# Optimization experiments

Measured on AMD Instinct MI355X. Metric: run time of the kernel, lower is better.

The kernel has to match this reference:

```python
import jax, jax.numpy as jnp
import numpy as np


def setup_inputs() -> dict:
    key = jax.random.key(0)
    x = jax.random.normal(key, (2_000_000, 9), dtype=jnp.float32)
    return {"x": x}


def reference(x):
    # Symmetric orthogonalization onto SO(3):
    #   M = U S V^T ;  R = U diag(1, 1, det(U V^T)) V^T
    m = x.reshape(-1, 3, 3)                      # [N, 3, 3]
    u, s, vh = jnp.linalg.svd(m, full_matrices=False)  # u:[N,3,3], vh:[N,3,3] (= V^T)
    det = jnp.linalg.det(jnp.matmul(u, vh))      # [N]
    # Flip last column of U by sign of det to land in SO(3) (det = +1)
    u_fixed = jnp.concatenate(
        [u[:, :, :2], u[:, :, 2:] * det[:, None, None]], axis=2
    )
    return jnp.matmul(u_fixed, vh)               # [N, 3, 3]
```

## Files before the change

kernel.cpp:

```cpp
#include <hip/hip_runtime.h>

#define TPB 256
#define MPW 128
#define FPW (MPW * 9)

typedef float v2f __attribute__((ext_vector_type(2)));
typedef int   v2i __attribute__((ext_vector_type(2)));

static __device__ __forceinline__ v2f sqrt2(v2f a){
    v2f r; r.x = __builtin_amdgcn_sqrtf(a.x); r.y = __builtin_amdgcn_sqrtf(a.y); return r;
}
static __device__ __forceinline__ v2f rsq2(v2f a){
    v2f r; r.x = __builtin_amdgcn_rsqf(a.x); r.y = __builtin_amdgcn_rsqf(a.y); return r;
}
static __device__ __forceinline__ v2f csign2(v2f x, v2f y){
    v2f r; r.x = copysignf(x.x, y.x); r.y = copysignf(x.y, y.y); return r;
}
static __device__ __forceinline__ v2f fabs2(v2f x){
    v2f r; r.x = fabsf(x.x); r.y = fabsf(x.y); return r;
}
static __device__ __forceinline__ v2f sel2(v2i m, v2f a, v2f b){
    v2f r; r.x = m.x ? a.x : b.x; r.y = m.y ? a.y : b.y; return r;
}
static __device__ __forceinline__ void rot2(v2f &p, v2f &q, v2f c, v2f s){
    v2f x = p, y = q; p = c*x - s*y; q = s*x + c*y;
}

static __device__ __forceinline__ void jrot2(v2f &app, v2f &aqq, v2f &apq,
                                             v2f &arp, v2f &arq,
                                             v2f &v0p, v2f &v1p, v2f &v2p,
                                             v2f &v0q, v2f &v1q, v2f &v2q)
{
    v2f d   = aqq - app;
    v2f w   = apq + apq;
    v2f nrm = d*d + w*w;
    v2f rr  = sqrt2(nrm);
    v2f sr  = csign2(rr, d);
    v2f den = d + sr;
    v2f inv = rsq2(den*den + w*w);
    v2f c   = fabs2(den) * inv;
    v2f s   = w * csign2(inv, den);
    v2i tiny = nrm < (v2f)1e-30f;
    c = sel2(tiny, (v2f)1.0f, c);
    s = sel2(tiny, (v2f)0.0f, s);
    v2f sum = app + aqq;
    v2f lo  = 0.5f*(sum - sr);
    app = lo; aqq = sum - lo; apq = (v2f)0.0f;
    rot2(arp, arq, c, s);
    rot2(v0p, v0q, c, s);
    rot2(v1p, v1q, c, s);
    rot2(v2p, v2q, c, s);
}

static __device__ __forceinline__ void solve2(
    v2f m00, v2f m01, v2f m02,
    v2f m10, v2f m11, v2f m12,
    v2f m20, v2f m21, v2f m22,
    v2f &r00, v2f &r01, v2f &r02,
    v2f &r10, v2f &r11, v2f &r12,
    v2f &r20, v2f &r21, v2f &r22)
{
    v2f a00 = m00*m00 + m10*m10 + m20*m20;
    v2f a11 = m01*m01 + m11*m11 + m21*m21;
    v2f a22 = m02*m02 + m12*m12 + m22*m22;
    v2f a01 = m00*m01 + m10*m11 + m20*m21;
    v2f a02 = m00*m02 + m10*m12 + m20*m22;
    v2f a12 = m01*m02 + m11*m12 + m21*m22;

    v2f v00 = (v2f)1.0f, v01 = (v2f)0.0f, v02 = (v2f)0.0f;
    v2f v10 = (v2f)0.0f, v11 = (v2f)1.0f, v12 = (v2f)0.0f;
    v2f v20 = (v2f)0.0f, v21 = (v2f)0.0f, v22 = (v2f)1.0f;

    #pragma unroll
    for (int sw = 0; sw < 3; ++sw) {
        jrot2(a00, a11, a01, a02, a12, v00, v10, v20, v01, v11, v21);
        jrot2(a00, a22, a02, a01, a12, v00, v10, v20, v02, v12, v22);
        jrot2(a11, a22, a12, a01, a02, v01, v11, v21, v02, v12, v22);
    }

    v2f t;
    {
        v2i c01 = a00 < a11;
        t = a00; a00 = sel2(c01, a11, a00); a11 = sel2(c01, t, a11);
        t = v00; v00 = sel2(c01, v01, v00); v01 = sel2(c01, -t, v01);
        t = v10; v10 = sel2(c01, v11, v10); v11 = sel2(c01, -t, v11);
        t = v20; v20 = sel2(c01, v21, v20); v21 = sel2(c01, -t, v21);
    }
    {
        v2i c02 = a00 < a22;
        t = a00; a00 = sel2(c02, a22, a00); a22 = sel2(c02, t, a22);
        t = v00; v00 = sel2(c02, v02, v00); v02 = sel2(c02, -t, v02);
        t = v10; v10 = sel2(c02, v12, v10); v12 = sel2(c02, -t, v12);
        t = v20; v20 = sel2(c02, v22, v20); v22 = sel2(c02, -t, v22);
    }
    {
        v2i c12 = a11 < a22;
        t = a11; a11 = sel2(c12, a22, a11); a22 = sel2(c12, t, a22);
        t = v01; v01 = sel2(c12, v02, v01); v02 = sel2(c12, -t, v02);
        t = v11; v11 = sel2(c12, v12, v11); v12 = sel2(c12, -t, v12);
        t = v21; v21 = sel2(c12, v22, v21); v22 = sel2(c12, -t, v22);
    }

    v2f b00 = m00*v00 + m01*v10 + m02*v20;
    v2f b10 = m10*v00 + m11*v10 + m12*v20;
    v2f b20 = m20*v00 + m21*v10 + m22*v20;
    v2f b01 = m00*v01 + m01*v11 + m02*v21;
    v2f b11 = m10*v01 + m11*v11 + m12*v21;
    v2f b21 = m20*v01 + m21*v11 + m22*v21;

    v2f n1 = b00*b00 + b10*b10 + b20*b20;
    v2f i1 = rsq2(n1);
    v2i ok1 = n1 > (v2f)1e-30f;
    i1 = sel2(ok1, i1, (v2f)0.0f);
    v2f u00 = b00*i1, u10 = b10*i1, u20 = b20*i1;

    v2f d12 = b01*u00 + b11*u10 + b21*u20;
    v2f q0 = b01 - d12*u00;
    v2f q1 = b11 - d12*u10;
    v2f q2 = b21 - d12*u20;
    v2f n2 = q0*q0 + q1*q1 + q2*q2;
    v2f i2 = rsq2(n2);
    v2i ok2 = n2 > (v2f)1e-30f;
    i2 = sel2(ok2, i2, (v2f)0.0f);
    v2f u01 = q0*i2, u11 = q1*i2, u21 = q2*i2;

    v2f u02 = u10*u21 - u20*u11;
    v2f u12 = u20*u01 - u00*u21;
    v2f u22 = u00*u11 - u10*u01;

    r00 = u00*v00 + u01*v01 + u02*v02;
    r01 = u00*v10 + u01*v11 + u02*v12;
    r02 = u00*v20 + u01*v21 + u02*v22;
    r10 = u10*v00 + u11*v01 + u12*v02;
    r11 = u10*v10 + u11*v11 + u12*v12;
    r12 = u10*v20 + u11*v21 + u12*v22;
    r20 = u20*v00 + u21*v01 + u22*v02;
    r21 = u20*v10 + u21*v11 + u22*v12;
    r22 = u20*v20 + u21*v21 + u22*v22;
}

static __device__ __forceinline__ float4 ld_f4(const float* __restrict__ x, long f, long ntotf){
    if (f + 4 <= ntotf) return *(const float4*)(x + f);
    float4 r = make_float4(0.f, 0.f, 0.f, 0.f);
    if (f     < ntotf) r.x = x[f];
    if (f + 1 < ntotf) r.y = x[f + 1];
    if (f + 2 < ntotf) r.z = x[f + 2];
    if (f + 3 < ntotf) r.w = x[f + 3];
    return r;
}
static __device__ __forceinline__ void st_f4(float* __restrict__ o, long f, float4 v, long ntotf){
    if (f + 4 <= ntotf) { *(float4*)(o + f) = v; return; }
    if (f     < ntotf) o[f]     = v.x;
    if (f + 1 < ntotf) o[f + 1] = v.y;
    if (f + 2 < ntotf) o[f + 2] = v.z;
    if (f + 3 < ntotf) o[f + 3] = v.w;
}

__global__ __launch_bounds__(TPB) void svdo_kernel(const float* __restrict__ x,
                                                   float* __restrict__ out,
                                                   int nmat, int ntiles, int W)
{
    __shared__ float lds[4][FPW];
    const int lane = threadIdx.x & 63;
    const int wv   = threadIdx.x >> 6;
    const long ntotf = (long)nmat * 9;

    int tile = blockIdx.x * 4 + wv;
    if (tile >= ntiles) return;

    float* L = lds[wv];

    float4 q0, q1, q2, q3, q4;
    {
        const long fb = (long)tile * FPW;
        q0 = ld_f4(x, fb + (long)(lane       ) * 4, ntotf);
        q1 = ld_f4(x, fb + (long)(lane +  64) * 4, ntotf);
        q2 = ld_f4(x, fb + (long)(lane + 128) * 4, ntotf);
        q3 = ld_f4(x, fb + (long)(lane + 192) * 4, ntotf);
        q4 = make_float4(0.f, 0.f, 0.f, 0.f);
        if (lane < 32) q4 = ld_f4(x, fb + (long)(lane + 256) * 4, ntotf);
    }

    for (;;) {
        *(float4*)&L[(lane       ) * 4] = q0;
        *(float4*)&L[(lane +  64) * 4] = q1;
        *(float4*)&L[(lane + 128) * 4] = q2;
        *(float4*)&L[(lane + 192) * 4] = q3;
        if (lane < 32) *(float4*)&L[(lane + 256) * 4] = q4;
        asm volatile("s_waitcnt lgkmcnt(0)" ::: "memory");

        const int  nxt  = tile + W;
        const bool have = nxt < ntiles;
        if (have) {
            const long fb = (long)nxt * FPW;
            q0 = ld_f4(x, fb + (long)(lane       ) * 4, ntotf);
            q1 = ld_f4(x, fb + (long)(lane +  64) * 4, ntotf);
            q2 = ld_f4(x, fb + (long)(lane + 128) * 4, ntotf);
            q3 = ld_f4(x, fb + (long)(lane + 192) * 4, ntotf);
            if (lane < 32) q4 = ld_f4(x, fb + (long)(lane + 256) * 4, ntotf);
        }

        {
            const float* p0 = &L[lane * 9];
            const float* p1 = &L[(lane + 64) * 9];
            v2f m00 = {p0[0], p1[0]}, m01 = {p0[1], p1[1]}, m02 = {p0[2], p1[2]};
            v2f m10 = {p0[3], p1[3]}, m11 = {p0[4], p1[4]}, m12 = {p0[5], p1[5]};
            v2f m20 = {p0[6], p1[6]}, m21 = {p0[7], p1[7]}, m22 = {p0[8], p1[8]};

            v2f r00, r01, r02, r10, r11, r12, r20, r21, r22;
            solve2(m00, m01, m02, m10, m11, m12, m20, m21, m22,
                   r00, r01, r02, r10, r11, r12, r20, r21, r22);

            float* o0 = &L[lane * 9];
            o0[0]=r00.x; o0[1]=r01.x; o0[2]=r02.x;
            o0[3]=r10.x; o0[4]=r11.x; o0[5]=r12.x;
            o0[6]=r20.x; o0[7]=r21.x; o0[8]=r22.x;
            float* o1 = &L[(lane + 64) * 9];
            o1[0]=r00.y; o1[1]=r01.y; o1[2]=r02.y;
            o1[3]=r10.y; o1[4]=r11.y; o1[5]=r12.y;
            o1[6]=r20.y; o1[7]=r21.y; o1[8]=r22.y;
        }
        asm volatile("s_waitcnt lgkmcnt(0)" ::: "memory");

        {
            const long fb = (long)tile * FPW;
            st_f4(out, fb + (long)(lane       ) * 4, *(const float4*)&L[(lane       ) * 4], ntotf);
            st_f4(out, fb + (long)(lane +  64) * 4, *(const float4*)&L[(lane +  64) * 4], ntotf);
            st_f4(out, fb + (long)(lane + 128) * 4, *(const float4*)&L[(lane + 128) * 4], ntotf);
            st_f4(out, fb + (long)(lane + 192) * 4, *(const float4*)&L[(lane + 192) * 4], ntotf);
            if (lane < 32)
                st_f4(out, fb + (long)(lane + 256) * 4, *(const float4*)&L[(lane + 256) * 4], ntotf);
        }

        if (!have) break;
        tile = nxt;
    }
}

extern "C" void kernel_launch(void* const* d_in, const int* in_sizes, int n_in,
                              void* d_out, int out_size, void* d_ws, size_t ws_size,
                              hipStream_t stream)
{
    (void)n_in; (void)d_ws; (void)ws_size; (void)out_size;
    const float* x = (const float*)d_in[0];
    float* out = (float*)d_out;
    const int nmat = in_sizes[0] / 9;
    const int ntiles = (nmat + MPW - 1) / MPW;
    int grid = (ntiles + 3) / 4;
    if (grid > 1536) grid = 1536;
    const int W = grid * 4;
    svdo_kernel<<<grid, TPB, 0, stream>>>(x, out, nmat, ntiles, W);
}
```

Baseline: 33.06 us.

## Double-buffer input tiles via global_load_lds DMA and add tail path

Replaces register-staged loads followed by LDS writes with direct global-to-LDS DMA (global_load_lds) into a per-wave double buffer, prefetching the next tile while the current one is solved. A separate scalar path handles the partial final tile, so the bounds-checked vector load and store helpers go away. The grid cap is lowered from 1536 to 1024 blocks, and the LDS footprint doubles. The waitcnt-based synchronisation is delicate: vmcnt(5) assumes a specific ordering of the outstanding loads and stores, which risks races.

```diff
diff --git a/kernel.cpp b/kernel.cpp
--- a/kernel.cpp
+++ b/kernel.cpp
@@ -2,10 +2,20 @@
 
 #define TPB 256
 #define MPW 128
-#define FPW (MPW * 9)
+#define FPT (MPW * 9)
 
 typedef float v2f __attribute__((ext_vector_type(2)));
 typedef int   v2i __attribute__((ext_vector_type(2)));
+
+typedef __attribute__((address_space(1))) const void gv_t;
+typedef __attribute__((address_space(3))) void lv_t;
+
+static __device__ __forceinline__ void dma16(const float* g, float* l){
+    __builtin_amdgcn_global_load_lds((gv_t*)g, (lv_t*)l, 16, 0, 0);
+}
+static __device__ __forceinline__ void dma4(const float* g, float* l){
+    __builtin_amdgcn_global_load_lds((gv_t*)g, (lv_t*)l, 4, 0, 0);
+}
 
 static __device__ __forceinline__ v2f sqrt2(v2f a){
     v2f r; r.x = __builtin_amdgcn_sqrtf(a.x); r.y = __builtin_amdgcn_sqrtf(a.y); return r;
@@ -139,101 +149,129 @@
     r22 = u20*v20 + u21*v21 + u22*v22;
 }
 
-static __device__ __forceinline__ float4 ld_f4(const float* __restrict__ x, long f, long ntotf){
-    if (f + 4 <= ntotf) return *(const float4*)(x + f);
-    float4 r = make_float4(0.f, 0.f, 0.f, 0.f);
-    if (f     < ntotf) r.x = x[f];
-    if (f + 1 < ntotf) r.y = x[f + 1];
-    if (f + 2 < ntotf) r.z = x[f + 2];
-    if (f + 3 < ntotf) r.w = x[f + 3];
-    return r;
-}
-static __device__ __forceinline__ void st_f4(float* __restrict__ o, long f, float4 v, long ntotf){
-    if (f + 4 <= ntotf) { *(float4*)(o + f) = v; return; }
-    if (f     < ntotf) o[f]     = v.x;
-    if (f + 1 < ntotf) o[f + 1] = v.y;
-    if (f + 2 < ntotf) o[f + 2] = v.z;
-    if (f + 3 < ntotf) o[f + 3] = v.w;
-}
-
 __global__ __launch_bounds__(TPB) void svdo_kernel(const float* __restrict__ x,
                                                    float* __restrict__ out,
                                                    int nmat, int ntiles, int W)
 {
-    __shared__ float lds[4][FPW];
+    __shared__ float lds[4][2][FPT];
     const int lane = threadIdx.x & 63;
     const int wv   = threadIdx.x >> 6;
-    const long ntotf = (long)nmat * 9;
 
     int tile = blockIdx.x * 4 + wv;
     if (tile >= ntiles) return;
 
-    float* L = lds[wv];
-
-    float4 q0, q1, q2, q3, q4;
-    {
-        const long fb = (long)tile * FPW;
-        q0 = ld_f4(x, fb + (long)(lane       ) * 4, ntotf);
-        q1 = ld_f4(x, fb + (long)(lane +  64) * 4, ntotf);
-        q2 = ld_f4(x, fb + (long)(lane + 128) * 4, ntotf);
-        q3 = ld_f4(x, fb + (long)(lane + 192) * 4, ntotf);
-        q4 = make_float4(0.f, 0.f, 0.f, 0.f);
-        if (lane < 32) q4 = ld_f4(x, fb + (long)(lane + 256) * 4, ntotf);
-    }
-
-    for (;;) {
-        *(float4*)&L[(lane       ) * 4] = q0;
-        *(float4*)&L[(lane +  64) * 4] = q1;
-        *(float4*)&L[(lane + 128) * 4] = q2;
-        *(float4*)&L[(lane + 192) * 4] = q3;
-        if (lane < 32) *(float4*)&L[(lane + 256) * 4] = q4;
+    int cur = 0;
+    bool full = (long)(tile + 1) * MPW <= (long)nmat;
+
+    if (full) {
+        {
+            const long fb = (long)tile * FPT;
+            float* D = lds[wv][0];
+            dma16(x + fb +        lane * 4, &D[0]);
+            dma16(x + fb +  256 + lane * 4, &D[256]);
+            dma16(x + fb +  512 + lane * 4, &D[512]);
+            dma16(x + fb +  768 + lane * 4, &D[768]);
+            dma4 (x + fb + 1024 + lane,     &D[1024]);
+            dma4 (x + fb + 1088 + lane,     &D[1088]);
+            asm volatile("s_waitcnt vmcnt(0)" ::: "memory");
+        }
+
+        for (;;) {
+            const int  nxt   = tile + W;
+            const bool have  = nxt < ntiles;
+            const bool nfull = have && ((long)(nxt + 1) * MPW <= (long)nmat);
+
+            if (nfull) {
+                const long fb = (long)nxt * FPT;
+                float* D = lds[wv][cur ^ 1];
+                dma16(x + fb +        lane * 4, &D[0]);
+                dma16(x + fb +  256 + lane * 4, &D[256]);
+                dma16(x + fb +  512 + lane * 4, &D[512]);
+                dma16(x + fb +  768 + lane * 4, &D[768]);
+                dma4 (x + fb + 1024 + lane,     &D[1024]);
+                dma4 (x + fb + 1088 + lane,     &D[1088]);
+            }
+
+            float* L = lds[wv][cur];
+            {
+                const float* p0 = &L[lane * 9];
+                const float* p1 = &L[(lane + 64) * 9];
+                v2f m00 = {p0[0], p1[0]}, m01 = {p0[1], p1[1]}, m02 = {p0[2], p1[2]};
+                v2f m10 = {p0[3], p1[3]}, m11 = {p0[4], p1[4]}, m12 = {p0[5], p1[5]};
+                v2f m20 = {p0[6], p1[6]}, m21 = {p0[7], p1[7]}, m22 = {p0[8], p1[8]};
+
+                v2f r00, r01, r02, r10, r11, r12, r20, r21, r22;
+                solve2(m00, m01, m02, m10, m11, m12, m20, m21, m22,
+                       r00, r01, r02, r10, r11, r12, r20, r21, r22);
+
+                float* o0 = &L[lane * 9];
+                o0[0]=r00.x; o0[1]=r01.x; o0[2]=r02.x;
+                o0[3]=r10.x; o0[4]=r11.x; o0[5]=r12.x;
+                o0[6]=r20.x; o0[7]=r21.x; o0[8]=r22.x;
+                float* o1 = &L[(lane + 64) * 9];
+                o1[0]=r00.y; o1[1]=r01.y; o1[2]=r02.y;
+                o1[3]=r10.y; o1[4]=r11.y; o1[5]=r12.y;
+                o1[6]=r20.y; o1[7]=r21.y; o1[8]=r22.y;
+            }
+            asm volatile("" ::: "memory");
+
+            {
+                const long fb = (long)tile * FPT;
+                float4 s0 = *(const float4*)&L[(lane       ) * 4];
+                float4 s1 = *(const float4*)&L[(lane +  64) * 4];
+                float4 s2 = *(const float4*)&L[(lane + 128) * 4];
+                float4 s3 = *(const float4*)&L[(lane + 192) * 4];
+                *(float4*)(out + fb + (lane       ) * 4) = s0;
+                *(float4*)(out + fb + (lane +  64) * 4) = s1;
+                *(float4*)(out + fb + (lane + 128) * 4) = s2;
+                *(float4*)(out + fb + (lane + 192) * 4) = s3;
+                if (lane < 32) {
+                    float4 s4 = *(const float4*)&L[(lane + 256) * 4];
+                    *(float4*)(out + fb + (lane + 256) * 4) = s4;
+                }
+            }
+
+            asm volatile("s_waitcnt vmcnt(5)" ::: "memory");
+
+            if (!have) return;
+            tile = nxt;
+            if (!nfull) break;
+            cur ^= 1;
+        }
+    }
+
+    {
+        const long ntotf = (long)nmat * 9;
+        const long fb = (long)tile * FPT;
+        float* L = lds[wv][0];
+        for (int idx = lane; idx < FPT; idx += 64) {
+            long f = fb + idx;
+            L[idx] = (f < ntotf) ? x[f] : 0.0f;
+        }
+        asm volatile("s_waitcnt vmcnt(0) lgkmcnt(0)" ::: "memory");
+
+        const float* p0 = &L[lane * 9];
+        const float* p1 = &L[(lane + 64) * 9];
+        v2f m00 = {p0[0], p1[0]}, m01 = {p0[1], p1[1]}, m02 = {p0[2], p1[2]};
+        v2f m10 = {p0[3], p1[3]}, m11 = {p0[4], p1[4]}, m12 = {p0[5], p1[5]};
+        v2f m20 = {p0[6], p1[6]}, m21 = {p0[7], p1[7]}, m22 = {p0[8], p1[8]};
+        v2f r00, r01, r02, r10, r11, r12, r20, r21, r22;
+        solve2(m00, m01, m02, m10, m11, m12, m20, m21, m22,
+               r00, r01, r02, r10, r11, r12, r20, r21, r22);
+        float* o0 = &L[lane * 9];
+        o0[0]=r00.x; o0[1]=r01.x; o0[2]=r02.x;
+        o0[3]=r10.x; o0[4]=r11.x; o0[5]=r12.x;
+        o0[6]=r20.x; o0[7]=r21.x; o0[8]=r22.x;
+        float* o1 = &L[(lane + 64) * 9];
+        o1[0]=r00.y; o1[1]=r01.y; o1[2]=r02.y;
+        o1[3]=r10.y; o1[4]=r11.y; o1[5]=r12.y;
+        o1[6]=r20.y; o1[7]=r21.y; o1[8]=r22.y;
         asm volatile("s_waitcnt lgkmcnt(0)" ::: "memory");
 
-        const int  nxt  = tile + W;
-        const bool have = nxt < ntiles;
-        if (have) {
-            const long fb = (long)nxt * FPW;
-            q0 = ld_f4(x, fb + (long)(lane       ) * 4, ntotf);
-            q1 = ld_f4(x, fb + (long)(lane +  64) * 4, ntotf);
-            q2 = ld_f4(x, fb + (long)(lane + 128) * 4, ntotf);
-            q3 = ld_f4(x, fb + (long)(lane + 192) * 4, ntotf);
-            if (lane < 32) q4 = ld_f4(x, fb + (long)(lane + 256) * 4, ntotf);
-        }
-
-        {
-            const float* p0 = &L[lane * 9];
-            const float* p1 = &L[(lane + 64) * 9];
-            v2f m00 = {p0[0], p1[0]}, m01 = {p0[1], p1[1]}, m02 = {p0[2], p1[2]};
-            v2f m10 = {p0[3], p1[3]}, m11 = {p0[4], p1[4]}, m12 = {p0[5], p1[5]};
-            v2f m20 = {p0[6], p1[6]}, m21 = {p0[7], p1[7]}, m22 = {p0[8], p1[8]};
-
-            v2f r00, r01, r02, r10, r11, r12, r20, r21, r22;
-            solve2(m00, m01, m02, m10, m11, m12, m20, m21, m22,
-                   r00, r01, r02, r10, r11, r12, r20, r21, r22);
-
-            float* o0 = &L[lane * 9];
-            o0[0]=r00.x; o0[1]=r01.x; o0[2]=r02.x;
-            o0[3]=r10.x; o0[4]=r11.x; o0[5]=r12.x;
-            o0[6]=r20.x; o0[7]=r21.x; o0[8]=r22.x;
-            float* o1 = &L[(lane + 64) * 9];
-            o1[0]=r00.y; o1[1]=r01.y; o1[2]=r02.y;
-            o1[3]=r10.y; o1[4]=r11.y; o1[5]=r12.y;
-            o1[6]=r20.y; o1[7]=r21.y; o1[8]=r22.y;
-        }
-        asm volatile("s_waitcnt lgkmcnt(0)" ::: "memory");
-
-        {
-            const long fb = (long)tile * FPW;
-            st_f4(out, fb + (long)(lane       ) * 4, *(const float4*)&L[(lane       ) * 4], ntotf);
-            st_f4(out, fb + (long)(lane +  64) * 4, *(const float4*)&L[(lane +  64) * 4], ntotf);
-            st_f4(out, fb + (long)(lane + 128) * 4, *(const float4*)&L[(lane + 128) * 4], ntotf);
-            st_f4(out, fb + (long)(lane + 192) * 4, *(const float4*)&L[(lane + 192) * 4], ntotf);
-            if (lane < 32)
-                st_f4(out, fb + (long)(lane + 256) * 4, *(const float4*)&L[(lane + 256) * 4], ntotf);
-        }
-
-        if (!have) break;
-        tile = nxt;
+        for (int idx = lane; idx < FPT; idx += 64) {
+            long f = fb + idx;
+            if (f < ntotf) out[f] = L[idx];
+        }
     }
 }
 
@@ -247,7 +285,7 @@
     const int nmat = in_sizes[0] / 9;
     const int ntiles = (nmat + MPW - 1) / MPW;
     int grid = (ntiles + 3) / 4;
-    if (grid > 1536) grid = 1536;
+    if (grid > 1024) grid = 1024;
     const int W = grid * 4;
     svdo_kernel<<<grid, TPB, 0, stream>>>(x, out, nmat, ntiles, W);
 }
```

Measured after the change: 32.05 us. 1.03x faster.
